# Kernel optimization log

Hardware: AMD Instinct MI355X
Metric: run time of the kernel (lower is better)

Reference implementation:

```python
import jax, jax.numpy as jnp
import numpy as np

MARGIN = 0.5
EPS = 1e-6  # torch F.pairwise_distance adds eps to the difference: ||x1 - x2 + eps||

B, C, D = 262144, 100, 128


def setup_inputs() -> dict:
    key = jax.random.key(0)
    k1, k2, k3 = jax.random.split(key, 3)
    features = jax.random.normal(k1, (B, D), dtype=jnp.float32)
    prototypes = jax.random.normal(k2, (C, D), dtype=jnp.float32)
    labels = jax.random.randint(k3, (B,), 0, C, dtype=jnp.int64)
    return {"features": features, "prototypes": prototypes, "labels": labels}


def _l2_normalize(x, axis=-1, eps=1e-12):
    # matches torch F.normalize: x / max(||x||, eps)
    n = jnp.sqrt(jnp.sum(x * x, axis=axis, keepdims=True))
    return x / jnp.maximum(n, eps)


def reference(features, prototypes, labels):
    f = _l2_normalize(features, axis=1)        # [B, D]
    p = _l2_normalize(prototypes, axis=1)      # [C, D]
    Bn, Dn = f.shape
    Cn = p.shape[0]

    # ||f_i - p_j + EPS||^2 = ||f_i||^2 + ||p_j||^2 - 2 f_i.p_j
    #                         + 2*EPS*(sum(f_i) - sum(p_j)) + D*EPS^2
    dot = f @ p.T                              # [B, C]
    f2 = jnp.sum(f * f, axis=1)                # [B]
    p2 = jnp.sum(p * p, axis=1)                # [C]
    sf = jnp.sum(f, axis=1)                    # [B]
    sp = jnp.sum(p, axis=1)                    # [C]
    d2 = (f2[:, None] + p2[None, :] - 2.0 * dot
          + 2.0 * EPS * (sf[:, None] - sp[None, :])
          + Dn * (EPS * EPS))                  # [B, C]
    dists = jnp.sqrt(jnp.maximum(d2, 1e-12))   # [B, C]

    d_pos = jnp.take_along_axis(dists, labels[:, None], axis=1)  # [B, 1]
    hinge = jax.nn.relu(d_pos - dists + MARGIN)                  # [B, C]
    neg_mask = jnp.arange(Cn)[None, :] != labels[:, None]        # [B, C]
    # per-sample mean over the C-1 negative prototypes, then mean over batch
    per_sample = jnp.sum(jnp.where(neg_mask, hinge, 0.0), axis=1) / (Cn - 1)
    return jnp.mean(per_sample)
```

## Files before the change

### kernel.cpp

```cpp
#include <hip/hip_runtime.h>
#include <hip/hip_bf16.h>
#include <math.h>

#define DD 128
#define CC 100
#define NPAD 112
#define NT 7
#define MARGIN_F 0.5f
#define EPS_F 1e-6f
#define RW 16
#define CH 4
#define BROWS 256
#define NFRAG (NT * 4)

typedef __attribute__((ext_vector_type(8))) short bf16x8;
typedef __attribute__((ext_vector_type(4))) float f32x4;

__device__ __forceinline__ float fsqrt_f(float x) { return __builtin_amdgcn_sqrtf(x); }
__device__ __forceinline__ float frcp_f(float x)  { return __builtin_amdgcn_rcpf(x); }

__device__ __forceinline__ short f2bf(float x) {
    __hip_bfloat16 h = __float2bfloat16(x);
    return *reinterpret_cast<short*>(&h);
}

__global__ void prep_kernel(const float* __restrict__ p,
                            float* __restrict__ cj,
                            bf16x8* __restrict__ pnb,
                            float* __restrict__ out) {
    int j = blockIdx.x, tid = threadIdx.x;
    if (j == 0 && tid == 0) out[0] = -MARGIN_F / (float)(CC - 1);

    float inv = 0.0f;
    if (j < CC) {
        float a = p[j * DD + tid];
        float b = p[j * DD + tid + 64];
        float ss = a * a + b * b;
        float s1 = a + b;
#pragma unroll
        for (int off = 1; off < 64; off <<= 1) {
            ss += __shfl_xor(ss, off);
            s1 += __shfl_xor(s1, off);
        }
        inv = 1.0f / fmaxf(sqrtf(ss), 1e-12f);
        if (tid == 0) cj[j] = ss * inv * inv - 2.0f * EPS_F * (s1 * inv);
    } else {
        if (tid == 0) cj[j] = 1e9f;
    }

    if (tid < 16) {
        int kk = tid >> 2, g = tid & 3;
        int frag = (j >> 4) * 4 + kk;
        int lane = g * 16 + (j & 15);
        bf16x8 o;
        if (j < CC) {
            const float* row = p + j * DD + kk * 32 + g * 8;
#pragma unroll
            for (int q = 0; q < 8; ++q) o[q] = f2bf(row[q] * inv);
        } else {
#pragma unroll
            for (int q = 0; q < 8; ++q) o[q] = 0;
        }
        pnb[frag * 64 + lane] = o;
    }
}

__global__ __launch_bounds__(256) void proto_main_kernel(
        const float* __restrict__ feat,
        const bf16x8* __restrict__ pnb,
        const float* __restrict__ cj,
        const int* __restrict__ labels,
        float* __restrict__ out,
        int Bn, float scale) {
    const int lane = threadIdx.x & 63;
    const int w = threadIdx.x >> 6;
    const int g = lane >> 4, m = lane & 15;
    const long blkbase = (long)blockIdx.x * BROWS;

    __shared__ bf16x8 pnl[NFRAG * 64];
    __shared__ float red[4];

    float cjr[NT];
#pragma unroll
    for (int t = 0; t < NT; ++t) cjr[t] = cj[t * 16 + m];

    float4 va[8];
    int lab;
    {
        long row = blkbase + w * RW + m;
        long rs = row < Bn ? row : (long)(Bn - 1);
        lab = labels[rs];
        const float4* fp = (const float4*)(feat + rs * DD);
#pragma unroll
        for (int kk = 0; kk < 4; ++kk) {
            va[kk * 2]     = fp[kk * 8 + g * 2];
            va[kk * 2 + 1] = fp[kk * 8 + g * 2 + 1];
        }
    }

#pragma unroll
    for (int i = 0; i < NFRAG * 64 / 256; ++i)
        pnl[i * 256 + threadIdx.x] = pnb[i * 256 + threadIdx.x];
    __syncthreads();

    float hsum = 0.f;

#pragma unroll
    for (int c = 0; c < CH; ++c) {
        float ss = 0.f, s1 = 0.f;
#pragma unroll
        for (int q = 0; q < 8; ++q) {
            float4 v = va[q];
            ss += v.x * v.x + v.y * v.y + v.z * v.z + v.w * v.w;
            s1 += v.x + v.y + v.z + v.w;
        }
        ss += __shfl_xor(ss, 16); ss += __shfl_xor(ss, 32);
        s1 += __shfl_xor(s1, 16); s1 += __shfl_xor(s1, 32);
        float inv = frcp_f(fmaxf(fsqrt_f(ss), 1e-12f));
        float cf = ss * inv * inv + 2.f * EPS_F * (s1 * inv)
                 + (float)DD * (EPS_F * EPS_F);
        float m2i = -2.f * inv;
        int labc = lab;

        bf16x8 afr[4];
#pragma unroll
        for (int kk = 0; kk < 4; ++kk) {
            float4 a = va[kk * 2], b = va[kk * 2 + 1];
            union { bf16x8 v; __hip_bfloat162 h[4]; } u;
            u.h[0] = __float22bfloat162_rn(make_float2(a.x, a.y));
            u.h[1] = __float22bfloat162_rn(make_float2(a.z, a.w));
            u.h[2] = __float22bfloat162_rn(make_float2(b.x, b.y));
            u.h[3] = __float22bfloat162_rn(make_float2(b.z, b.w));
            afr[kk] = u.v;
        }

        if (c + 1 < CH) {
            long nrow = blkbase + (c + 1) * 64 + w * RW + m;
            long nrs = nrow < Bn ? nrow : (long)(Bn - 1);
            lab = labels[nrs];
            const float4* fp = (const float4*)(feat + nrs * DD);
#pragma unroll
            for (int kk = 0; kk < 4; ++kk) {
                va[kk * 2]     = fp[kk * 8 + g * 2];
                va[kk * 2 + 1] = fp[kk * 8 + g * 2 + 1];
            }
        }

        f32x4 acc[NT];
#pragma unroll
        for (int t = 0; t < NT; ++t) acc[t] = (f32x4)0.f;
#pragma unroll
        for (int t = 0; t < NT; ++t) {
            bf16x8 bfr[4];
#pragma unroll
            for (int kk = 0; kk < 4; ++kk) bfr[kk] = pnl[(t * 4 + kk) * 64 + lane];
#pragma unroll
            for (int kk = 0; kk < 4; ++kk)
                acc[t] = __builtin_amdgcn_mfma_f32_16x16x32_bf16(
                    afr[kk], bfr[kk], acc[t], 0, 0, 0);
        }

        float cf_r[4], m2i_r[4];
        int lab_r[4];
#pragma unroll
        for (int r = 0; r < 4; ++r) {
            int addr = (g * 4 + r) << 2;
            cf_r[r]  = __int_as_float(__builtin_amdgcn_ds_bpermute(addr, __float_as_int(cf)));
            m2i_r[r] = __int_as_float(__builtin_amdgcn_ds_bpermute(addr, __float_as_int(m2i)));
            lab_r[r] = __builtin_amdgcn_ds_bpermute(addr, labc);
        }

        float dsel[4] = {0.f, 0.f, 0.f, 0.f};
#pragma unroll
        for (int t = 0; t < NT; ++t) {
            int col = t * 16 + m;
#pragma unroll
            for (int r = 0; r < 4; ++r) {
                float d2 = fmaf(acc[t][r], m2i_r[r], cf_r[r] + cjr[t]);
                float dist = fsqrt_f(fmaxf(d2, 1e-12f));
                acc[t][r] = dist;
                dsel[r] = (lab_r[r] == col) ? dist : dsel[r];
            }
        }

        float hb[4];
#pragma unroll
        for (int r = 0; r < 4; ++r) {
            int sl = ((g << 4) + (lab_r[r] & 15)) << 2;
            float dp = __int_as_float(__builtin_amdgcn_ds_bpermute(sl, __float_as_int(dsel[r])));
            long rr = blkbase + c * 64 + w * RW + g * 4 + r;
            hb[r] = (rr < (long)Bn) ? (dp + MARGIN_F) : -1e30f;
        }

#pragma unroll
        for (int t = 0; t < NT; ++t)
#pragma unroll
            for (int r = 0; r < 4; ++r)
                hsum += fmaxf(hb[r] - acc[t][r], 0.f);
    }

#pragma unroll
    for (int off = 32; off > 0; off >>= 1) hsum += __shfl_xor(hsum, off);
    if (lane == 0) red[w] = hsum;
    __syncthreads();
    if (threadIdx.x == 0)
        atomicAdd(out, (red[0] + red[1] + red[2] + red[3]) * scale);
}

extern "C" void kernel_launch(void* const* d_in, const int* in_sizes, int n_in,
                              void* d_out, int out_size, void* d_ws, size_t ws_size,
                              hipStream_t stream) {
    const float* feat   = (const float*)d_in[0];
    const float* prot   = (const float*)d_in[1];
    const int*   labels = (const int*)d_in[2];
    float* out = (float*)d_out;
    int Bn = in_sizes[0] / DD;

    bf16x8* pnb = (bf16x8*)d_ws;
    float* cjw  = (float*)((char*)d_ws + 28 * 64 * 16);

    prep_kernel<<<NPAD, 64, 0, stream>>>(prot, cjw, pnb, out);

    int blocks = (Bn + BROWS - 1) / BROWS;
    float scale = 1.0f / ((float)Bn * (float)(CC - 1));
    proto_main_kernel<<<blocks, 256, 0, stream>>>(feat, pnb, cjw, labels, out, Bn, scale);
}
```

Baseline: 42.17 us.

## Compute positive distance with a dedicated MFMA and rewrite hinge as min-sum

Before the full distance tile, the positive-class distance is now computed from an extra 4-MFMA pass that gathers the label's prototype fragment, plus an LDS copy of the per-class constants. This removes the per-element label compare/select and one bpermute from the main loop. The hinge relu(hb - d) is then rewritten as hb - min(d, hb), summed as NT*hb - sum(min), which drops the clamp before the sqrt and the separate relu pass. The cost is extra MFMA work and bpermutes per chunk. Padded columns rely on the large cj value to contribute zero.

```diff
diff --git a/kernel.cpp b/kernel.cpp
--- a/kernel.cpp
+++ b/kernel.cpp
@@ -78,6 +78,7 @@
     const long blkbase = (long)blockIdx.x * BROWS;
 
     __shared__ bf16x8 pnl[NFRAG * 64];
+    __shared__ float cjs[NPAD];
     __shared__ float red[4];
 
     float cjr[NT];
@@ -101,6 +102,7 @@
 #pragma unroll
     for (int i = 0; i < NFRAG * 64 / 256; ++i)
         pnl[i * 256 + threadIdx.x] = pnb[i * 256 + threadIdx.x];
+    if (threadIdx.x < NPAD) cjs[threadIdx.x] = cj[threadIdx.x];
     __syncthreads();
 
     float hsum = 0.f;
@@ -146,20 +148,6 @@
             }
         }
 
-        f32x4 acc[NT];
-#pragma unroll
-        for (int t = 0; t < NT; ++t) acc[t] = (f32x4)0.f;
-#pragma unroll
-        for (int t = 0; t < NT; ++t) {
-            bf16x8 bfr[4];
-#pragma unroll
-            for (int kk = 0; kk < 4; ++kk) bfr[kk] = pnl[(t * 4 + kk) * 64 + lane];
-#pragma unroll
-            for (int kk = 0; kk < 4; ++kk)
-                acc[t] = __builtin_amdgcn_mfma_f32_16x16x32_bf16(
-                    afr[kk], bfr[kk], acc[t], 0, 0, 0);
-        }
-
         float cf_r[4], m2i_r[4];
         int lab_r[4];
 #pragma unroll
@@ -169,34 +157,69 @@
             m2i_r[r] = __int_as_float(__builtin_amdgcn_ds_bpermute(addr, __float_as_int(m2i)));
             lab_r[r] = __builtin_amdgcn_ds_bpermute(addr, labc);
         }
-
-        float dsel[4] = {0.f, 0.f, 0.f, 0.f};
+        float cjl_r[4];
+#pragma unroll
+        for (int r = 0; r < 4; ++r) cjl_r[r] = cjs[lab_r[r]];
+
+        f32x4 accpos = (f32x4)0.f;
+        {
+            int lanehi = lane & 48;
+            int fbase = (labc >> 4) << 2;
+            int lsub  = lanehi + (labc & 15);
+#pragma unroll
+            for (int kk = 0; kk < 4; ++kk) {
+                bf16x8 bp = pnl[(fbase + kk) * 64 + lsub];
+                accpos = __builtin_amdgcn_mfma_f32_16x16x32_bf16(
+                    afr[kk], bp, accpos, 0, 0, 0);
+            }
+        }
+        float a01 = (lane & 1) ? accpos[1] : accpos[0];
+        float a23 = (lane & 1) ? accpos[3] : accpos[2];
+        float vsrc = (lane & 2) ? a23 : a01;
+        float hb[4];
+        {
+            int hl = (lane >> 4) * 20;
+#pragma unroll
+            for (int r = 0; r < 4; ++r) {
+                float dotp = __int_as_float(
+                    __builtin_amdgcn_ds_bpermute((hl + r) << 2, __float_as_int(vsrc)));
+                float d2p = fmaf(dotp, m2i_r[r], cf_r[r]) + cjl_r[r];
+                float dpd = fsqrt_f(fmaxf(d2p, 1e-12f));
+                long rr = blkbase + c * 64 + w * RW + g * 4 + r;
+                hb[r] = (rr < (long)Bn) ? (dpd + MARGIN_F) : 0.f;
+            }
+        }
+
+        f32x4 acc[NT];
+#pragma unroll
+        for (int t = 0; t < NT; ++t) acc[t] = (f32x4)0.f;
 #pragma unroll
         for (int t = 0; t < NT; ++t) {
-            int col = t * 16 + m;
-#pragma unroll
-            for (int r = 0; r < 4; ++r) {
-                float d2 = fmaf(acc[t][r], m2i_r[r], cf_r[r] + cjr[t]);
-                float dist = fsqrt_f(fmaxf(d2, 1e-12f));
-                acc[t][r] = dist;
-                dsel[r] = (lab_r[r] == col) ? dist : dsel[r];
-            }
-        }
-
-        float hb[4];
-#pragma unroll
-        for (int r = 0; r < 4; ++r) {
-            int sl = ((g << 4) + (lab_r[r] & 15)) << 2;
-            float dp = __int_as_float(__builtin_amdgcn_ds_bpermute(sl, __float_as_int(dsel[r])));
-            long rr = blkbase + c * 64 + w * RW + g * 4 + r;
-            hb[r] = (rr < (long)Bn) ? (dp + MARGIN_F) : -1e30f;
-        }
-
-#pragma unroll
-        for (int t = 0; t < NT; ++t)
-#pragma unroll
-            for (int r = 0; r < 4; ++r)
-                hsum += fmaxf(hb[r] - acc[t][r], 0.f);
+            bf16x8 bfr[4];
+#pragma unroll
+            for (int kk = 0; kk < 4; ++kk) bfr[kk] = pnl[(t * 4 + kk) * 64 + lane];
+#pragma unroll
+            for (int kk = 0; kk < 4; ++kk)
+                acc[t] = __builtin_amdgcn_mfma_f32_16x16x32_bf16(
+                    afr[kk], bfr[kk], acc[t], 0, 0, 0);
+        }
+
+        float ms0 = 0.f, ms1 = 0.f, ms2 = 0.f, ms3 = 0.f;
+#pragma unroll
+        for (int t = 0; t < NT; ++t) {
+            float e0 = fmaf(acc[t][0], m2i_r[0], cf_r[0]);
+            float e1 = fmaf(acc[t][1], m2i_r[1], cf_r[1]);
+            float e2 = fmaf(acc[t][2], m2i_r[2], cf_r[2]);
+            float e3 = fmaf(acc[t][3], m2i_r[3], cf_r[3]);
+            ms0 += fminf(fsqrt_f(e0 + cjr[t]), hb[0]);
+            ms1 += fminf(fsqrt_f(e1 + cjr[t]), hb[1]);
+            ms2 += fminf(fsqrt_f(e2 + cjr[t]), hb[2]);
+            ms3 += fminf(fsqrt_f(e3 + cjr[t]), hb[3]);
+        }
+        hsum += fmaf((float)NT, hb[0], -ms0);
+        hsum += fmaf((float)NT, hb[1], -ms1);
+        hsum += fmaf((float)NT, hb[2], -ms2);
+        hsum += fmaf((float)NT, hb[3], -ms3);
     }
 
 #pragma unroll
```

Result: faster. 40.03 us (-5.1%).
